# Performance work log

Measured on AMD Instinct MI355X. Metric: run time of the kernel, lower is better.

## Reference

```python
import jax, jax.numpy as jnp
import numpy as np

NUM_CLASSES = 80


def _bce_logits(x, y):
    # numerically stable BCEWithLogits, elementwise
    return jnp.maximum(x, 0.0) - x * y + jnp.log1p(jnp.exp(-jnp.abs(x)))


def _iou_center(b1, b2):
    # boxes in (cx, cy, w, h) format, last dim = 4; returns IoU, last dim dropped
    b1x1 = b1[..., 0] - b1[..., 2] / 2
    b1y1 = b1[..., 1] - b1[..., 3] / 2
    b1x2 = b1[..., 0] + b1[..., 2] / 2
    b1y2 = b1[..., 1] + b1[..., 3] / 2
    b2x1 = b2[..., 0] - b2[..., 2] / 2
    b2y1 = b2[..., 1] - b2[..., 3] / 2
    b2x2 = b2[..., 0] + b2[..., 2] / 2
    b2y2 = b2[..., 1] + b2[..., 3] / 2
    iw = jnp.clip(jnp.minimum(b1x2, b2x2) - jnp.maximum(b1x1, b2x1), 0.0)
    ih = jnp.clip(jnp.minimum(b1y2, b2y2) - jnp.maximum(b1y1, b2y1), 0.0)
    inter = iw * ih
    union = (b1x2 - b1x1) * (b1y2 - b1y1) + (b2x2 - b2x1) * (b2y2 - b2y1) - inter
    return inter / (union + 1e-16)


def setup_inputs() -> dict:
    key = jax.random.key(0)
    kp, ko, kxy, kwh, kc, ka = jax.random.split(key, 6)
    B, A, S = 32, 3, 52
    predictions = jax.random.normal(kp, (B, A, S, S, 5 + NUM_CLASSES), dtype=jnp.float32)
    obj_flag = jax.random.bernoulli(ko, 0.3, (B, A, S, S, 1)).astype(jnp.float32)
    xy = jax.random.uniform(kxy, (B, A, S, S, 2), dtype=jnp.float32)
    wh = jax.random.uniform(kwh, (B, A, S, S, 2), minval=0.05, maxval=1.5, dtype=jnp.float32)
    cls = jax.random.randint(kc, (B, A, S, S, 1), 0, NUM_CLASSES).astype(jnp.float32)
    target = jnp.concatenate([obj_flag, xy, wh, cls], axis=-1)
    anchors = jax.random.uniform(ka, (3, 2), minval=0.1, maxval=1.0, dtype=jnp.float32)
    return {"predictions": predictions, "target": target, "anchors": anchors}


def reference(predictions, target, anchors):
    obj = (target[..., 0] == 1).astype(predictions.dtype)    # [B,3,S,S]
    noobj = (target[..., 0] == 0).astype(predictions.dtype)  # [B,3,S,S]
    n_obj = jnp.sum(obj)
    n_noobj = jnp.sum(noobj)

    anchors_r = anchors.reshape(1, 3, 1, 1, 2)
    pred_obj = predictions[..., 0]
    tgt_obj = target[..., 0]

    # noobj BCE (masked mean over noobj cells)
    no_detection = jnp.sum(_bce_logits(pred_obj, tgt_obj) * noobj) / n_noobj

    # decoded boxes and IoU (detached)
    pred_xy = jax.nn.sigmoid(predictions[..., 1:3])
    pred_wh_dec = jnp.exp(predictions[..., 3:5]) * anchors_r
    box_preds = jnp.concatenate([pred_xy, pred_wh_dec], axis=-1)
    ious = jax.lax.stop_gradient(_iou_center(box_preds, target[..., 1:5]))  # [B,3,S,S]

    # obj BCE against IoU-scaled targets (masked mean over obj cells)
    detection = jnp.sum(_bce_logits(pred_obj, ious * tgt_obj) * obj) / n_obj

    # box MSE: sigmoid(xy) & raw wh vs target xy & log(wh/anchors)
    pred_box = jnp.concatenate([pred_xy, predictions[..., 3:5]], axis=-1)
    tgt_box = jnp.concatenate(
        [target[..., 1:3], jnp.log(1e-16 + target[..., 3:5] / anchors_r)], axis=-1)
    box = jnp.sum(((pred_box - tgt_box) ** 2) * obj[..., None]) / (4.0 * n_obj)

    # classification CE (masked mean over obj cells)
    logp = jax.nn.log_softmax(predictions[..., 5:], axis=-1)
    labels = target[..., 5].astype(jnp.int32)
    nll = -jnp.take_along_axis(logp, labels[..., None], axis=-1)[..., 0]
    classification = jnp.sum(nll * obj) / n_obj

    return box + detection + no_detection + classification
```

## Files before the change

### kernel.cpp

```cpp
#include <hip/hip_runtime.h>

#define TILE      64
#define NTHREADS  256
#define STRIDE    85
#define SSPAN     2704
#define MAXGRID   2028
#define PF4       ((TILE*STRIDE)/4)
#define TF4       ((TILE*6)/4)

__device__ __forceinline__ float wave_reduce(float v) {
    #pragma unroll
    for (int off = 32; off > 0; off >>= 1)
        v += __shfl_down(v, off, 64);
    return v;
}

__global__ __launch_bounds__(NTHREADS) void loss_partial(
    const float* __restrict__ pred, const float* __restrict__ tgt,
    const float* __restrict__ anchors, float* __restrict__ partial,
    int n_full, int n_rem)
{
    __shared__ float lds_p[TILE * STRIDE];
    __shared__ float lds_t[TILE * 6];
    __shared__ float red[4][6];

    const int tid    = threadIdx.x;
    const int lane   = tid & 63;
    const int wid    = tid >> 6;
    const int cell_l = tid >> 2;
    const int part   = tid & 3;

    const float aw0 = anchors[0], ah0 = anchors[1];
    const float aw1 = anchors[2], ah1 = anchors[3];
    const float aw2 = anchors[4], ah2 = anchors[5];

    float a_obj = 0.f, a_nobj = 0.f, a_bceo = 0.f, a_bceno = 0.f,
          a_box = 0.f, a_cls = 0.f;

    float4 rp[6];
    float4 rt;

    auto prefetch = [&](int t) {
        const float4* gp = (const float4*)(pred + (size_t)t * (TILE * STRIDE));
        #pragma unroll
        for (int j = 0; j < 5; ++j) rp[j] = gp[tid + j * NTHREADS];
        if (tid < PF4 - 5 * NTHREADS) rp[5] = gp[tid + 5 * NTHREADS];
        const float4* gt = (const float4*)(tgt + (size_t)t * (TILE * 6));
        if (tid < TF4) rt = gt[tid];
    };
    auto stow = [&]() {
        float4* lp = (float4*)lds_p;
        #pragma unroll
        for (int j = 0; j < 5; ++j) lp[tid + j * NTHREADS] = rp[j];
        if (tid < PF4 - 5 * NTHREADS) lp[tid + 5 * NTHREADS] = rp[5];
        if (tid < TF4) ((float4*)lds_t)[tid] = rt;
    };

    int t = blockIdx.x;
    if (t < n_full) prefetch(t);

    for (; t < n_full; t += gridDim.x) {
        __syncthreads();
        stow();
        const int tn = t + gridDim.x;
        if (tn < n_full) prefetch(tn);
        __syncthreads();

        const float* cp = lds_p + cell_l * STRIDE + 5 + part * 20;
        float v[20];
        #pragma unroll
        for (int k = 0; k < 20; ++k) v[k] = cp[k];
        float mx = v[0];
        #pragma unroll
        for (int k = 1; k < 20; ++k) mx = fmaxf(mx, v[k]);
        mx = fmaxf(mx, __shfl_xor(mx, 1, 64));
        mx = fmaxf(mx, __shfl_xor(mx, 2, 64));
        float se = 0.f;
        #pragma unroll
        for (int k = 0; k < 20; ++k) se += __expf(v[k] - mx);
        se += __shfl_xor(se, 1, 64);
        se += __shfl_xor(se, 2, 64);

        if (part == 0) {
            const float* pc = lds_p + cell_l * STRIDE;
            const float* tc = lds_t + cell_l * 6;
            const float p0 = pc[0], t0 = tc[0];
            const float bce_base = fmaxf(p0, 0.f) + log1pf(__expf(-fabsf(p0)));
            if (t0 == 0.0f) { a_nobj += 1.f; a_bceno += bce_base; }
            if (t0 == 1.0f) {
                a_obj += 1.f;
                const int cell_g = t * TILE + cell_l;
                const int aidx = (cell_g / SSPAN) % 3;
                const float aw = aidx == 0 ? aw0 : (aidx == 1 ? aw1 : aw2);
                const float ah = aidx == 0 ? ah0 : (aidx == 1 ? ah1 : ah2);
                const float p1 = pc[1], p2 = pc[2], p3 = pc[3], p4 = pc[4];
                const float t1 = tc[1], t2 = tc[2], t3 = tc[3], t4 = tc[4];
                const float sx = 1.f / (1.f + __expf(-p1));
                const float sy = 1.f / (1.f + __expf(-p2));
                const float pw = __expf(p3) * aw, ph = __expf(p4) * ah;
                const float b1x1 = sx - pw * 0.5f, b1x2 = sx + pw * 0.5f;
                const float b1y1 = sy - ph * 0.5f, b1y2 = sy + ph * 0.5f;
                const float b2x1 = t1 - t3 * 0.5f, b2x2 = t1 + t3 * 0.5f;
                const float b2y1 = t2 - t4 * 0.5f, b2y2 = t2 + t4 * 0.5f;
                const float iw = fmaxf(fminf(b1x2, b2x2) - fmaxf(b1x1, b2x1), 0.f);
                const float ih = fmaxf(fminf(b1y2, b2y2) - fmaxf(b1y1, b2y1), 0.f);
                const float inter = iw * ih;
                const float uni = (b1x2 - b1x1) * (b1y2 - b1y1)
                                + (b2x2 - b2x1) * (b2y2 - b2y1) - inter;
                const float iou = inter / (uni + 1e-16f);
                a_bceo += bce_base - p0 * iou;
                const float lw = logf(1e-16f + t3 / aw);
                const float lh = logf(1e-16f + t4 / ah);
                const float d0 = sx - t1, d1 = sy - t2, d2 = p3 - lw, d3 = p4 - lh;
                a_box += d0 * d0 + d1 * d1 + d2 * d2 + d3 * d3;
                const int label = (int)tc[5];
                a_cls += (mx + __logf(se)) - pc[5 + label];
            }
        }
    }

    if (blockIdx.x == 0 && n_rem > 0 && cell_l < n_rem) {
        const int cell_g = n_full * TILE + cell_l;
        const float* cp = pred + (size_t)cell_g * STRIDE + 5 + part * 20;
        float v[20];
        #pragma unroll
        for (int k = 0; k < 20; ++k) v[k] = cp[k];
        float mx = v[0];
        #pragma unroll
        for (int k = 1; k < 20; ++k) mx = fmaxf(mx, v[k]);
        mx = fmaxf(mx, __shfl_xor(mx, 1, 64));
        mx = fmaxf(mx, __shfl_xor(mx, 2, 64));
        float se = 0.f;
        #pragma unroll
        for (int k = 0; k < 20; ++k) se += __expf(v[k] - mx);
        se += __shfl_xor(se, 1, 64);
        se += __shfl_xor(se, 2, 64);
        if (part == 0) {
            const float* pc = pred + (size_t)cell_g * STRIDE;
            const float* tc = tgt + (size_t)cell_g * 6;
            const float p0 = pc[0], t0 = tc[0];
            const float bce_base = fmaxf(p0, 0.f) + log1pf(__expf(-fabsf(p0)));
            if (t0 == 0.0f) { a_nobj += 1.f; a_bceno += bce_base; }
            if (t0 == 1.0f) {
                a_obj += 1.f;
                const int aidx = (cell_g / SSPAN) % 3;
                const float aw = aidx == 0 ? aw0 : (aidx == 1 ? aw1 : aw2);
                const float ah = aidx == 0 ? ah0 : (aidx == 1 ? ah1 : ah2);
                const float p1 = pc[1], p2 = pc[2], p3 = pc[3], p4 = pc[4];
                const float t1 = tc[1], t2 = tc[2], t3 = tc[3], t4 = tc[4];
                const float sx = 1.f / (1.f + __expf(-p1));
                const float sy = 1.f / (1.f + __expf(-p2));
                const float pw = __expf(p3) * aw, ph = __expf(p4) * ah;
                const float b1x1 = sx - pw * 0.5f, b1x2 = sx + pw * 0.5f;
                const float b1y1 = sy - ph * 0.5f, b1y2 = sy + ph * 0.5f;
                const float b2x1 = t1 - t3 * 0.5f, b2x2 = t1 + t3 * 0.5f;
                const float b2y1 = t2 - t4 * 0.5f, b2y2 = t2 + t4 * 0.5f;
                const float iw = fmaxf(fminf(b1x2, b2x2) - fmaxf(b1x1, b2x1), 0.f);
                const float ih = fmaxf(fminf(b1y2, b2y2) - fmaxf(b1y1, b2y1), 0.f);
                const float inter = iw * ih;
                const float uni = (b1x2 - b1x1) * (b1y2 - b1y1)
                                + (b2x2 - b2x1) * (b2y2 - b2y1) - inter;
                const float iou = inter / (uni + 1e-16f);
                a_bceo += bce_base - p0 * iou;
                const float lw = logf(1e-16f + t3 / aw);
                const float lh = logf(1e-16f + t4 / ah);
                const float d0 = sx - t1, d1 = sy - t2, d2 = p3 - lw, d3 = p4 - lh;
                a_box += d0 * d0 + d1 * d1 + d2 * d2 + d3 * d3;
                const int label = (int)tc[5];
                a_cls += (mx + __logf(se)) - pc[5 + label];
            }
        }
    }

    float vals[6] = {a_obj, a_nobj, a_bceo, a_bceno, a_box, a_cls};
    #pragma unroll
    for (int k = 0; k < 6; ++k) {
        const float r = wave_reduce(vals[k]);
        if (lane == 0) red[wid][k] = r;
    }
    __syncthreads();
    if (tid == 0) {
        #pragma unroll
        for (int k = 0; k < 6; ++k)
            partial[blockIdx.x * 6 + k] =
                red[0][k] + red[1][k] + red[2][k] + red[3][k];
    }
}

__global__ __launch_bounds__(NTHREADS) void loss_final(
    const float* __restrict__ partial, int nblocks, float* __restrict__ out)
{
    __shared__ float red[4][6];
    const int tid = threadIdx.x, lane = tid & 63, wid = tid >> 6;
    float s[6] = {0.f, 0.f, 0.f, 0.f, 0.f, 0.f};
    for (int i = tid; i < nblocks; i += NTHREADS) {
        #pragma unroll
        for (int k = 0; k < 6; ++k) s[k] += partial[i * 6 + k];
    }
    #pragma unroll
    for (int k = 0; k < 6; ++k) {
        const float r = wave_reduce(s[k]);
        if (lane == 0) red[wid][k] = r;
    }
    __syncthreads();
    if (tid == 0) {
        float t[6];
        #pragma unroll
        for (int k = 0; k < 6; ++k)
            t[k] = red[0][k] + red[1][k] + red[2][k] + red[3][k];
        const float n_obj = t[0], n_noobj = t[1];
        out[0] = t[2] / n_obj + t[3] / n_noobj
               + t[4] / (4.f * n_obj) + t[5] / n_obj;
    }
}

extern "C" void kernel_launch(void* const* d_in, const int* in_sizes, int n_in,
                              void* d_out, int out_size, void* d_ws, size_t ws_size,
                              hipStream_t stream) {
    const float* pred    = (const float*)d_in[0];
    const float* tgt     = (const float*)d_in[1];
    const float* anchors = (const float*)d_in[2];
    float* out = (float*)d_out;

    const int n_cells = in_sizes[1] / 6;
    const int n_full  = n_cells / TILE;
    const int n_rem   = n_cells % TILE;
    const int grid = n_full < MAXGRID ? (n_full > 0 ? n_full : 1) : MAXGRID;
    float* partial = (float*)d_ws;

    loss_partial<<<grid, NTHREADS, 0, stream>>>(pred, tgt, anchors, partial,
                                                n_full, n_rem);
    loss_final<<<1, NTHREADS, 0, stream>>>(partial, grid, out);
}
```

Before: 163.8 us.

## Stage tiles with direct global-to-LDS loads into a double buffer

Replaces the register-staged prefetch (global to registers, then registers to LDS) with __builtin_amdgcn_global_load_lds, which writes each tile straight into one of two LDS buffers. Explicit vmcnt waits and barriers let the next tile's load overlap compute on the current one. The grid is cut from 2028 to 768 blocks so each block loops over more tiles. LDS use roughly doubles, which may lower occupancy, and the hand-written waitcnt and barrier sequence is fragile.

```diff
diff --git a/kernel.cpp b/kernel.cpp
--- a/kernel.cpp
+++ b/kernel.cpp
@@ -4,15 +4,42 @@
 #define NTHREADS  256
 #define STRIDE    85
 #define SSPAN     2704
-#define MAXGRID   2028
-#define PF4       ((TILE*STRIDE)/4)
-#define TF4       ((TILE*6)/4)
+#define MAXGRID   768
+#define PRED_F4_T 1360
+#define TGT_F4_T  96
+#define TOT_F4    1456
+#define NCALLS    6
+#define SLOTS     (NCALLS*NTHREADS)
+#define BUF_FLOATS (SLOTS*4)
+#define LDS_T_OFF (PRED_F4_T*4)
+
+typedef __attribute__((address_space(1))) const void gas_void;
+typedef __attribute__((address_space(3))) void las_void;
 
 __device__ __forceinline__ float wave_reduce(float v) {
     #pragma unroll
     for (int off = 32; off > 0; off >>= 1)
         v += __shfl_down(v, off, 64);
     return v;
+}
+
+__device__ __forceinline__ void stage_tile(
+    const float* __restrict__ pred, const float* __restrict__ tgt,
+    int t, float* buf, int tid)
+{
+    const float* pbase = pred + (size_t)t * (TILE * STRIDE);
+    const float* tbase = tgt  + (size_t)t * (TILE * 6);
+    #pragma unroll
+    for (int c = 0; c < NCALLS; ++c) {
+        const int s = c * NTHREADS + tid;
+        const float* src;
+        if (s < PRED_F4_T)   src = pbase + (size_t)s * 4;
+        else if (s < TOT_F4) src = tbase + (size_t)(s - PRED_F4_T) * 4;
+        else                 src = tbase;
+        __builtin_amdgcn_global_load_lds((gas_void*)src,
+                                         (las_void*)(buf + (size_t)s * 4),
+                                         16, 0, 0);
+    }
 }
 
 __global__ __launch_bounds__(NTHREADS) void loss_partial(
@@ -20,8 +47,7 @@
     const float* __restrict__ anchors, float* __restrict__ partial,
     int n_full, int n_rem)
 {
-    __shared__ float lds_p[TILE * STRIDE];
-    __shared__ float lds_t[TILE * 6];
+    __shared__ float buf[2][BUF_FLOATS];
     __shared__ float red[4][6];
 
     const int tid    = threadIdx.x;
@@ -37,34 +63,23 @@
     float a_obj = 0.f, a_nobj = 0.f, a_bceo = 0.f, a_bceno = 0.f,
           a_box = 0.f, a_cls = 0.f;
 
-    float4 rp[6];
-    float4 rt;
-
-    auto prefetch = [&](int t) {
-        const float4* gp = (const float4*)(pred + (size_t)t * (TILE * STRIDE));
-        #pragma unroll
-        for (int j = 0; j < 5; ++j) rp[j] = gp[tid + j * NTHREADS];
-        if (tid < PF4 - 5 * NTHREADS) rp[5] = gp[tid + 5 * NTHREADS];
-        const float4* gt = (const float4*)(tgt + (size_t)t * (TILE * 6));
-        if (tid < TF4) rt = gt[tid];
-    };
-    auto stow = [&]() {
-        float4* lp = (float4*)lds_p;
-        #pragma unroll
-        for (int j = 0; j < 5; ++j) lp[tid + j * NTHREADS] = rp[j];
-        if (tid < PF4 - 5 * NTHREADS) lp[tid + 5 * NTHREADS] = rp[5];
-        if (tid < TF4) ((float4*)lds_t)[tid] = rt;
-    };
-
     int t = blockIdx.x;
-    if (t < n_full) prefetch(t);
-
-    for (; t < n_full; t += gridDim.x) {
-        __syncthreads();
-        stow();
-        const int tn = t + gridDim.x;
-        if (tn < n_full) prefetch(tn);
-        __syncthreads();
+    const int gstride = gridDim.x;
+    if (t < n_full) stage_tile(pred, tgt, t, buf[0], tid);
+    int cur = 0;
+
+    for (; t < n_full; t += gstride, cur ^= 1) {
+        const int tn = t + gstride;
+        if (tn < n_full) {
+            stage_tile(pred, tgt, tn, buf[cur ^ 1], tid);
+            asm volatile("s_waitcnt vmcnt(6)" ::: "memory");
+        } else {
+            asm volatile("s_waitcnt vmcnt(0)" ::: "memory");
+        }
+        __builtin_amdgcn_s_barrier();
+
+        const float* lds_p = buf[cur];
+        const float* lds_t = buf[cur] + LDS_T_OFF;
 
         const float* cp = lds_p + cell_l * STRIDE + 5 + part * 20;
         float v[20];
@@ -117,6 +132,8 @@
                 a_cls += (mx + __logf(se)) - pc[5 + label];
             }
         }
+        asm volatile("" ::: "memory");
+        __builtin_amdgcn_s_barrier();
     }
 
     if (blockIdx.x == 0 && n_rem > 0 && cell_l < n_rem) {
@@ -225,7 +242,8 @@
     const int n_cells = in_sizes[1] / 6;
     const int n_full  = n_cells / TILE;
     const int n_rem   = n_cells % TILE;
-    const int grid = n_full < MAXGRID ? (n_full > 0 ? n_full : 1) : MAXGRID;
+    int grid = n_full < MAXGRID ? n_full : MAXGRID;
+    if (grid < 1) grid = 1;
     float* partial = (float*)d_ws;
 
     loss_partial<<<grid, NTHREADS, 0, stream>>>(pred, tgt, anchors, partial,
```

Result: faster. 143.0 us (-12.7%).
